# Optimization experiments

Hardware: AMD Instinct MI355X
Metric: run time of the kernel (lower is better)

The kernel has to match this reference:

```python
import jax, jax.numpy as jnp
import numpy as np

B, T, E, H, K, V = 64, 256, 300, 500, 64, 32000  # batch, seq, embed, hidden/dir, tags, vocab
PAD, EOS, SOS = 0, 1, 2
NEG = -10000.0


def setup_inputs() -> dict:
    key = jax.random.key(0)
    ks = jax.random.split(key, 20)
    rn = lambda k, shape, s=0.05: jax.random.normal(k, shape, jnp.float32) * s
    inp = {}
    inp["x"] = jax.random.randint(ks[0], (B, T), 3, V)   # all > 0 -> mask all ones (no padding)
    inp["y0"] = jax.random.randint(ks[1], (B, T), 3, K)  # gold tags, avoid PAD/EOS/SOS
    inp["embed"] = rn(ks[2], (V, E), 0.1)
    dims = [E, 2 * H]  # layer-0 input = embed, layer-1 input = concat(bi-dir hidden)
    i = 3
    for l in (0, 1):
        for d in ("f", "b"):
            inp[f"Wih{l}{d}"] = rn(ks[i], (4 * H, dims[l])); i += 1
            inp[f"Whh{l}{d}"] = rn(ks[i], (4 * H, H)); i += 1
            inp[f"b{l}{d}"] = rn(ks[i], (4 * H,)); i += 1
    inp["Wout"] = rn(ks[i], (K, 2 * H))
    inp["bout"] = rn(ks[i + 1], (K,))
    tr = jax.random.normal(ks[i + 2], (K, K), jnp.float32)
    tr = (tr.at[SOS, :].set(NEG).at[:, EOS].set(NEG).at[:, PAD].set(NEG)
            .at[PAD, :].set(NEG).at[PAD, EOS].set(0.0).at[PAD, PAD].set(0.0))
    inp["trans"] = tr  # trans[next, prev]
    return inp


def _lstm_dir(xs, Wih, Whh, b, reverse):
    """xs: [T,B,D] -> [T,B,H]; PyTorch gate order i,f,g,o."""
    if reverse:
        xs = xs[::-1]
    z0 = jnp.zeros((xs.shape[1], Whh.shape[1]), xs.dtype)

    def step(carry, xt):
        h, c = carry
        z = xt @ Wih.T + h @ Whh.T + b
        i_, f_, g_, o_ = jnp.split(z, 4, axis=-1)
        c = jax.nn.sigmoid(f_) * c + jax.nn.sigmoid(i_) * jnp.tanh(g_)
        h = jax.nn.sigmoid(o_) * jnp.tanh(c)
        return (h, c), h

    _, hs = jax.lax.scan(step, (z0, z0), xs)
    return hs[::-1] if reverse else hs


def reference(x, y0, embed, Wih0f, Whh0f, b0f, Wih0b, Whh0b, b0b,
              Wih1f, Whh1f, b1f, Wih1b, Whh1b, b1b, Wout, bout, trans):
    xs = embed[x].transpose(1, 0, 2)  # [T,B,E]
    h0 = jnp.concatenate([_lstm_dir(xs, Wih0f, Whh0f, b0f, False),
                          _lstm_dir(xs, Wih0b, Whh0b, b0b, True)], axis=-1)
    h1 = jnp.concatenate([_lstm_dir(h0, Wih1f, Whh1f, b1f, False),
                          _lstm_dir(h0, Wih1b, Whh1b, b1b, True)], axis=-1)
    emit = h1 @ Wout.T + bout                  # [T,B,K]
    mask = (x > 0).astype(emit.dtype).T        # [T,B]
    emit = emit * mask[..., None]              # y = y * mask

    # CRF partition (forward algorithm): new[b,j] = LSE_i(score[b,i] + trans[j,i]) + emit[t,b,j]
    init = jnp.full((B, K), NEG, emit.dtype).at[:, SOS].set(0.0)

    def step(score, em):
        e_t, m_t = em
        new = jax.nn.logsumexp(score[:, None, :] + trans[None, :, :], axis=-1) + e_t
        return jnp.where(m_t[:, None] > 0, new, score), None

    final, _ = jax.lax.scan(step, init, (emit, mask))
    Z = jax.nn.logsumexp(final, axis=-1)       # [B]

    # gold path score
    tags = jnp.concatenate([jnp.full((B, 1), SOS, y0.dtype), y0], axis=1)  # [B,T+1]
    e = jnp.take_along_axis(emit.transpose(1, 0, 2), tags[:, 1:, None], axis=2)[..., 0]  # [B,T]
    tr = trans[tags[:, 1:], tags[:, :-1]] * mask.T                                       # [B,T]
    gold = (e + tr).sum(axis=1)
    return Z - gold
```

## Files before the change

kernel.cpp:

```cpp
#include <hip/hip_runtime.h>
#include <hip/hip_bf16.h>

typedef short bf16x4 __attribute__((ext_vector_type(4)));
typedef short bf16x8 __attribute__((ext_vector_type(8)));
typedef float f32x4 __attribute__((ext_vector_type(4)));
typedef __hip_bfloat16 bf16;
typedef unsigned long long ull;

#define NEGV -10000.0f


__device__ __forceinline__ float sigm(float v) { return 1.0f / (1.0f + __expf(-v)); }
__device__ __forceinline__ float tanh_(float v) { float e = __expf(2.0f * v); return 1.0f - 2.0f / (e + 1.0f); }

__device__ __forceinline__ void async_load16(const bf16* g, const char* l) {
  __builtin_amdgcn_global_load_lds((const __attribute__((address_space(1))) void*)g,
                                   (__attribute__((address_space(3))) void*)l, 16, 0, 0);
}


__global__ __launch_bounds__(256) void pack_w0(const float* __restrict__ wf, const float* __restrict__ wb,
                                               bf16* __restrict__ dst) {
  int idx = blockIdx.x * 256 + threadIdx.x;
  int u = idx & 7, lane = (idx >> 3) & 63, rem = idx >> 9;
  int kt = rem % 10, nt = rem / 10;
  int n = (nt << 4) + (lane & 15), k = (kt << 5) + ((lane >> 4) << 3) + u;
  int d = n >> 11, g = (n >> 9) & 3, j = n & 511;
  float v = 0.f;
  if (j < 500 && k < 300) v = (d ? wb : wf)[(g * 500 + j) * 300 + k];
  dst[idx] = __float2bfloat16(v);
}

__global__ __launch_bounds__(256) void pack_whh4(const float* __restrict__ w0f, const float* __restrict__ w0b,
                                                 const float* __restrict__ w1f, const float* __restrict__ w1b,
                                                 bf16* __restrict__ dst) {
  const int which = blockIdx.y;
  const float* w = which == 0 ? w0f : which == 1 ? w0b : which == 2 ? w1f : w1b;
  int idx = blockIdx.x * 256 + threadIdx.x;
  int u = idx & 7, lane = (idx >> 3) & 63, rem = idx >> 9;
  int kt = rem & 15, nt = rem >> 4;
  int n = (nt << 4) + (lane & 15), k = (kt << 5) + ((lane >> 4) << 3) + u;
  int g = n >> 9, j = n & 511;
  float v = 0.f;
  if (j < 500 && k < 500) v = w[(g * 500 + j) * 500 + k];
  dst[(size_t)which * 1048576 + idx] = __float2bfloat16(v);
}

__global__ __launch_bounds__(256) void pack_w1(const float* __restrict__ wf, const float* __restrict__ wb,
                                               bf16* __restrict__ dst) {
  int idx = blockIdx.x * 256 + threadIdx.x;
  int u = idx & 7, lane = (idx >> 3) & 63, rem = idx >> 9;
  int kt = rem & 31, nt = rem >> 5;
  int n = (nt << 4) + (lane & 15), k = (kt << 5) + ((lane >> 4) << 3) + u;
  int d = n >> 11, g = (n >> 9) & 3, j = n & 511;
  int kk = k & 511;
  int ks = (k < 512) ? kk : 500 + kk;
  float v = 0.f;
  if (j < 500 && kk < 500) v = (d ? wb : wf)[(g * 500 + j) * 1000 + ks];
  dst[idx] = __float2bfloat16(v);
}

__global__ __launch_bounds__(256) void pack_wout(const float* __restrict__ w, bf16* __restrict__ dst) {
  int idx = blockIdx.x * 256 + threadIdx.x;
  int u = idx & 7, lane = (idx >> 3) & 63, rem = idx >> 9;
  int kt = rem & 31, nt = rem >> 5;
  int n = (nt << 4) + (lane & 15), k = (kt << 5) + ((lane >> 4) << 3) + u;
  int kk = k & 511;
  int ks = (k < 512) ? kk : 500 + kk;
  float v = 0.f;
  if (kk < 500) v = w[n * 1000 + ks];
  dst[idx] = __float2bfloat16(v);
}

__global__ __launch_bounds__(256) void pack_bias2(const float* __restrict__ b0f, const float* __restrict__ b0b,
                                                  const float* __restrict__ b1f, const float* __restrict__ b1b,
                                                  float* __restrict__ dst0, float* __restrict__ dst1) {
  int idx = blockIdx.x * 256 + threadIdx.x;
  int layer = idx >> 12, w = idx & 4095;
  int d = w >> 11, g = (w >> 9) & 3, j = w & 511;
  const float* src = layer ? (d ? b1b : b1f) : (d ? b0b : b0f);
  float v = (j < 500) ? src[g * 500 + j] : 0.f;
  (layer ? dst1 : dst0)[w] = v;
}

__global__ __launch_bounds__(256) void embed_k(const int* __restrict__ x, const float* __restrict__ em,
                                               bf16* __restrict__ xs) {
  int idx = blockIdx.x * 256 + threadIdx.x;
  int e = idx % 320;
  int row = idx / 320;
  int t = row >> 6, b = row & 63;
  float v = 0.f;
  if (e < 300) {
    int xv = x[b * 256 + t];
    v = em[(size_t)xv * 300 + e];
  }
  xs[idx] = __float2bfloat16(v);
}

__global__ __launch_bounds__(256) void gemm_nt(const bf16* __restrict__ A, const bf16* __restrict__ Bf,
                                               bf16* __restrict__ C, int Kdim, int Kt) {
  const int lane = threadIdx.x & 63, wave = threadIdx.x >> 6;
  const int lr = lane & 15, lh = lane >> 4;
  const int mb = blockIdx.x * 64;
  const int ntb = blockIdx.y * 16 + wave * 4;
  f32x4 acc[4][4] = {};
  for (int kt = 0; kt < Kt; ++kt) {
    bf16x8 a[4], b[4];
#pragma unroll
    for (int mt = 0; mt < 4; ++mt)
      a[mt] = *(const bf16x8*)(A + (size_t)(mb + mt * 16 + lr) * Kdim + kt * 32 + lh * 8);
#pragma unroll
    for (int q = 0; q < 4; ++q)
      b[q] = *(const bf16x8*)(Bf + ((size_t)(ntb + q) * Kt + kt) * 512 + lane * 8);
#pragma unroll
    for (int mt = 0; mt < 4; ++mt)
#pragma unroll
      for (int q = 0; q < 4; ++q)
        acc[mt][q] = __builtin_amdgcn_mfma_f32_16x16x32_bf16(a[mt], b[q], acc[mt][q], 0, 0, 0);
  }
  const int t = blockIdx.x;
#pragma unroll
  for (int q = 0; q < 4; ++q) {
    const int colbase = (ntb + q) * 16;
    const int dirq = colbase >> 11, gq = (colbase >> 9) & 3, jbq = (colbase >> 4) & 31;
    unsigned short vals[16];
#pragma unroll
    for (int mt = 0; mt < 4; ++mt)
#pragma unroll
      for (int r = 0; r < 4; ++r) {
        bf16 hb = __float2bfloat16(acc[mt][q][r]);
        vals[mt * 4 + r] = *(unsigned short*)&hb;
      }
    bf16* outp = C + ((((size_t)t * 2 + dirq) * 32 + jbq) * 4 + gq) * 1024 + lane * 16;
    *(bf16x8*)(outp) = *(const bf16x8*)(vals);
    *(bf16x8*)(outp + 8) = *(const bf16x8*)(vals + 8);
  }
}

__global__ __launch_bounds__(256, 1) void lstm_pipe(const bf16* __restrict__ preP, const bf16* __restrict__ whh,
                                                    const float* __restrict__ bias, bf16* __restrict__ hout,
                                                    unsigned int* __restrict__ flags) {
  constexpr int ROWS = 16;
  const int tid = threadIdx.x, lane = tid & 63, wave = tid >> 6;
  const int lr = lane & 15, lh = lane >> 4;
  const int jb = blockIdx.x, dir = blockIdx.y, part = blockIdx.z;
  unsigned int* flg = flags + (dir * 4 + part) * 64;
  unsigned int* myflg = flg + jb;
  __shared__ __align__(64) char hlds[4][16][1024];
  __shared__ float xch[4 * ROWS * 17];
  __shared__ float cst[ROWS * 16];
  for (int i = tid; i < ROWS * 16; i += 256) cst[i] = 0.f;
  const float bb = bias[dir * 2048 + wave * 512 + jb * 16 + lr];
  const bf16* wbase = whh + ((size_t)(dir * 128 + wave * 32 + jb) * 16) * 512 + lane * 8;

  bf16x8 wfrag[16];
#pragma unroll
  for (int kt = 0; kt < 16; ++kt) wfrag[kt] = *(const bf16x8*)(wbase + kt * 512);

  unsigned short pf[4];
  {
    const int t0 = dir ? 255 : 0;
    *(bf16x4*)pf = *(const bf16x4*)(preP + ((((size_t)t0 * 2 + dir) * 32 + jb) * 4 + wave) * 1024 +
                                    lane * 16 + part * 4);
  }

  const int srow_st = lane >> 2, sq_st = lane & 3;
  const int gchunk = (sq_st + ((srow_st >> 1) & 3)) & 3;
  const int rp = (lh - ((lr >> 1) & 3)) & 3;

  for (int s = 0; s < 256; ++s) {
    const int t = dir ? 255 - s : s;
    f32x4 acc = {};
    if (s > 0) {
      const unsigned int tgt = (unsigned int)s;
      const int tp = dir ? t + 1 : t - 1;
      const bf16* hp = hout + (size_t)tp * 65536 + dir * 512 +
                       (size_t)(part * 16 + srow_st) * 1024 + gchunk * 8;
      unsigned int pend = 0xFFFFu;
      while (pend) {
        unsigned int v = __hip_atomic_load(flg + (lane & 31), __ATOMIC_RELAXED, __HIP_MEMORY_SCOPE_AGENT);
        unsigned int am = (unsigned int)__ballot((int)(v >= tgt));
        unsigned int ready = 0;
#pragma unroll
        for (int j = 0; j < 16; ++j) {
          if (((pend >> j) & 1u) && (((am >> (2 * j)) & 3u) == 3u)) {
            async_load16(hp + j * 32, (const char*)&hlds[wave][j][0] + lane * 16);
            ready |= 1u << j;
          }
        }
        if (ready) {
          asm volatile("s_waitcnt vmcnt(0)" ::: "memory");
#pragma unroll
          for (int j = 0; j < 16; ++j) {
            if ((ready >> j) & 1u) {
              const bf16x8 afr = *(const bf16x8*)(&hlds[wave][j][0] + lr * 64 + rp * 16);
              acc = __builtin_amdgcn_mfma_f32_16x16x32_bf16(afr, wfrag[j], acc, 0, 0, 0);
            }
          }
          pend &= ~ready;
        }
      }
    }
#pragma unroll
    for (int r = 0; r < 4; ++r) {
      bf16 pv; *(unsigned short*)&pv = pf[r];
      xch[(wave * ROWS + lh * 4 + r) * 17 + lr] = acc[r] + bb + __bfloat162float(pv);
    }
    __syncthreads();
    if (tid < ROWS * 8) {
      const int row = tid >> 3, c0 = (tid & 7) * 2;
      unsigned int pk = 0;
#pragma unroll
      for (int i = 0; i < 2; ++i) {
        int col = c0 + i;
        float gi = xch[(0 * ROWS + row) * 17 + col];
        float gf = xch[(1 * ROWS + row) * 17 + col];
        float gg = xch[(2 * ROWS + row) * 17 + col];
        float go = xch[(3 * ROWS + row) * 17 + col];
        float c = cst[row * 16 + col];
        float cn = sigm(gf) * c + sigm(gi) * tanh_(gg);
        cst[row * 16 + col] = cn;
        bf16 hb = __float2bfloat16(sigm(go) * tanh_(cn));
        pk |= (unsigned int)(*(unsigned short*)&hb) << (16 * i);
      }
      unsigned int* hq =
          (unsigned int*)(hout + ((size_t)t * 64 + part * ROWS + row) * 1024 + dir * 512 + jb * 16 + c0);
      __hip_atomic_store(hq, pk, __ATOMIC_RELAXED, __HIP_MEMORY_SCOPE_AGENT);
    }
    asm volatile("s_waitcnt vmcnt(0)" ::: "memory");
    __syncthreads();
    if (tid == 0)
      __hip_atomic_store(myflg, (unsigned int)(s + 1), __ATOMIC_RELAXED, __HIP_MEMORY_SCOPE_AGENT);
    if (s < 255) {
      const int tn = dir ? t - 1 : t + 1;
      *(bf16x4*)pf = *(const bf16x4*)(preP + ((((size_t)tn * 2 + dir) * 32 + jb) * 4 + wave) * 1024 +
                                      lane * 16 + part * 4);
    }
  }
}

__global__ __launch_bounds__(256) void emit_k(const bf16* __restrict__ h1, const bf16* __restrict__ wo,
                                              const float* __restrict__ bout, const int* __restrict__ x,
                                              float* __restrict__ emit) {
  const int tid = threadIdx.x, lane = tid & 63, wave = tid >> 6;
  const int lr = lane & 15, lh = lane >> 4;
  const int mb = blockIdx.x * 64 + wave * 16;
  f32x4 acc[4] = {};
  for (int kt = 0; kt < 32; ++kt) {
    bf16x8 a = *(const bf16x8*)(h1 + (size_t)(mb + lr) * 1024 + kt * 32 + lh * 8);
#pragma unroll
    for (int q = 0; q < 4; ++q) {
      bf16x8 b = *(const bf16x8*)(wo + ((size_t)(q * 32 + kt) * 64 + lane) * 8);
      acc[q] = __builtin_amdgcn_mfma_f32_16x16x32_bf16(a, b, acc[q], 0, 0, 0);
    }
  }
#pragma unroll
  for (int q = 0; q < 4; ++q)
#pragma unroll
    for (int r = 0; r < 4; ++r) {
      int row = mb + lh * 4 + r;
      int col = q * 16 + lr;
      int tt = row >> 6, bi = row & 63;
      float m = (x[bi * 256 + tt] > 0) ? 1.f : 0.f;
      emit[(size_t)row * 64 + col] = (acc[q][r] + bout[col]) * m;
    }
}

__global__ __launch_bounds__(256) void crf_k(const float* __restrict__ emit, const float* __restrict__ trans,
                                             const int* __restrict__ x, const int* __restrict__ y0,
                                             float* __restrict__ out) {
  const int b = blockIdx.x, tid = threadIdx.x;
  __shared__ float tr[4096];
  __shared__ float sc[2][64];
  __shared__ float pm[4][64], ps[4][64];
  __shared__ float redw[4];
  for (int i = tid; i < 4096; i += 256) tr[i] = trans[i];
  if (tid < 64) sc[0][tid] = (tid == 2) ? 0.f : NEGV;
  __syncthreads();
  {
    const int t = tid;
    const int tag = y0[b * 256 + t];
    const int prev = t ? y0[b * 256 + t - 1] : 2;
    const float m = (x[b * 256 + t] > 0) ? 1.f : 0.f;
    float g = emit[((size_t)t * 64 + b) * 64 + tag] + tr[tag * 64 + prev] * m;
    for (int o = 32; o; o >>= 1) g += __shfl_down(g, o, 64);
    if ((tid & 63) == 0) redw[tid >> 6] = g;
  }
  __syncthreads();
  const float gold = redw[0] + redw[1] + redw[2] + redw[3];
  const int j = tid & 63, kq = tid >> 6;
  int cur = 0;
  for (int t = 0; t < 256; ++t) {
    const float* trj = tr + j * 64 + kq * 16;
    const float* scc = sc[cur] + kq * 16;
    float v[16];
    float mx = -3.0e38f;
#pragma unroll
    for (int k = 0; k < 16; ++k) {
      v[k] = scc[k] + trj[k];
      mx = fmaxf(mx, v[k]);
    }
    float sm = 0.f;
#pragma unroll
    for (int k = 0; k < 16; ++k) sm += __expf(v[k] - mx);
    pm[kq][j] = mx;
    ps[kq][j] = sm;
    __syncthreads();
    if (kq == 0) {
      float M = fmaxf(fmaxf(pm[0][j], pm[1][j]), fmaxf(pm[2][j], pm[3][j]));
      float S = ps[0][j] * __expf(pm[0][j] - M) + ps[1][j] * __expf(pm[1][j] - M) +
                ps[2][j] * __expf(pm[2][j] - M) + ps[3][j] * __expf(pm[3][j] - M);
      float nv = M + __logf(S) + emit[((size_t)t * 64 + b) * 64 + j];
      sc[cur ^ 1][j] = (x[b * 256 + t] > 0) ? nv : sc[cur][j];
    }
    __syncthreads();
    cur ^= 1;
  }
  if (tid < 64) {
    float v2 = sc[cur][tid];
    float M = v2;
    for (int o = 32; o; o >>= 1) M = fmaxf(M, __shfl_xor(M, o, 64));
    float s2 = __expf(v2 - M);
    for (int o = 32; o; o >>= 1) s2 += __shfl_xor(s2, o, 64);
    if (tid == 0) out[b] = M + __logf(s2) - gold;
  }
}

extern "C" void kernel_launch(void* const* d_in, const int* in_sizes, int n_in, void* d_out, int out_size,
                              void* d_ws, size_t ws_size, hipStream_t stream) {
  (void)in_sizes; (void)n_in; (void)out_size; (void)ws_size;
  const int* x = (const int*)d_in[0];
  const int* y0 = (const int*)d_in[1];
  const float* embed = (const float*)d_in[2];
  const float* Wih0f = (const float*)d_in[3];
  const float* Whh0f = (const float*)d_in[4];
  const float* b0f = (const float*)d_in[5];
  const float* Wih0b = (const float*)d_in[6];
  const float* Whh0b = (const float*)d_in[7];
  const float* b0b = (const float*)d_in[8];
  const float* Wih1f = (const float*)d_in[9];
  const float* Whh1f = (const float*)d_in[10];
  const float* b1f = (const float*)d_in[11];
  const float* Wih1b = (const float*)d_in[12];
  const float* Whh1b = (const float*)d_in[13];
  const float* b1b = (const float*)d_in[14];
  const float* Wout = (const float*)d_in[15];
  const float* bout = (const float*)d_in[16];
  const float* trans = (const float*)d_in[17];

  char* p = (char*)d_ws;
  auto take = [&](size_t n) { char* r = p; p += (n + 255) & ~(size_t)255; return r; };
  unsigned int* flags = (unsigned int*)take(2048 * sizeof(unsigned int));
  bf16* xs = (bf16*)take(16384ull * 320 * 2);
  bf16* preP = (bf16*)take(16384ull * 4096 * 2);
  bf16* h0 = (bf16*)take(16384ull * 1024 * 2);
  bf16* h1 = (bf16*)take(16384ull * 1024 * 2);
  float* emitb = (float*)take(16384ull * 64 * 4);
  bf16* W0B = (bf16*)take(4096ull * 320 * 2);
  bf16* W1B = (bf16*)take(4096ull * 1024 * 2);
  bf16* WhhB = (bf16*)take(4ull * 1048576 * 2);
  bf16* WoB = (bf16*)take(64ull * 1024 * 2);
  float* bias0 = (float*)take(4096 * 4);
  float* bias1 = (float*)take(4096 * 4);

  hipMemsetAsync(flags, 0, 2048 * sizeof(unsigned int), stream);
  hipLaunchKernelGGL(pack_w0, dim3(5120), dim3(256), 0, stream, Wih0f, Wih0b, W0B);
  hipLaunchKernelGGL(pack_whh4, dim3(4096, 4), dim3(256), 0, stream, Whh0f, Whh0b, Whh1f, Whh1b, WhhB);
  hipLaunchKernelGGL(pack_w1, dim3(16384), dim3(256), 0, stream, Wih1f, Wih1b, W1B);
  hipLaunchKernelGGL(pack_wout, dim3(256), dim3(256), 0, stream, Wout, WoB);
  hipLaunchKernelGGL(pack_bias2, dim3(32), dim3(256), 0, stream, b0f, b0b, b1f, b1b, bias0, bias1);
  hipLaunchKernelGGL(embed_k, dim3(20480), dim3(256), 0, stream, x, embed, xs);

  hipLaunchKernelGGL(gemm_nt, dim3(256, 16), dim3(256), 0, stream, xs, W0B, preP, 320, 10);
  {
    const bf16* a0 = preP; const bf16* a1 = WhhB; const float* a2 = bias0; bf16* a3 = h0;
    unsigned int* a4 = flags;
    void* args[] = {&a0, &a1, &a2, &a3, &a4};
    hipLaunchCooperativeKernel((void*)lstm_pipe, dim3(32, 2, 4), dim3(256), args, 0, stream);
  }
  hipLaunchKernelGGL(gemm_nt, dim3(256, 16), dim3(256), 0, stream, h0, W1B, preP, 1024, 32);
  {
    const bf16* a0 = preP; const bf16* a1 = WhhB + 2ull * 1048576; const float* a2 = bias1; bf16* a3 = h1;
    unsigned int* a4 = flags + 1024;
    void* args[] = {&a0, &a1, &a2, &a3, &a4};
    hipLaunchCooperativeKernel((void*)lstm_pipe, dim3(32, 2, 4), dim3(256), args, 0, stream);
  }
  hipLaunchKernelGGL(emit_k, dim3(256), dim3(256), 0, stream, h1, WoB, bout, x, emitb);
  hipLaunchKernelGGL(crf_k, dim3(64), dim3(256), 0, stream, emitb, trans, x, y0, (float*)d_out);
}
```

Measured before the change: 2.574 ms.

## Restructure LSTM recurrence so each wave owns a batch part with all gates

The recurrent LSTM kernel now has each wave handle one batch quarter and compute all four gates, instead of each wave computing one gate and exchanging results through shared memory. The recurrent weights move from registers into LDS, shared by the four waves, and the grid shrinks from 256 to 64 blocks. This removes the per-step block barriers and shared-memory gate exchange, and the cell update runs in registers with per-wave flag publication. In exchange each wave issues four times the MFMAs and reads weights from LDS every step, and fewer CUs are used.

```diff
diff --git a/kernel.cpp b/kernel.cpp
--- a/kernel.cpp
+++ b/kernel.cpp
@@ -137,32 +137,40 @@
   }
 }
 
-__global__ __launch_bounds__(256, 1) void lstm_pipe(const bf16* __restrict__ preP, const bf16* __restrict__ whh,
-                                                    const float* __restrict__ bias, bf16* __restrict__ hout,
-                                                    unsigned int* __restrict__ flags) {
-  constexpr int ROWS = 16;
+__global__ __launch_bounds__(256, 1) void lstm_wav(const bf16* __restrict__ preP, const bf16* __restrict__ whh,
+                                                   const float* __restrict__ bias, bf16* __restrict__ hout,
+                                                   unsigned int* __restrict__ flags) {
   const int tid = threadIdx.x, lane = tid & 63, wave = tid >> 6;
   const int lr = lane & 15, lh = lane >> 4;
-  const int jb = blockIdx.x, dir = blockIdx.y, part = blockIdx.z;
+  const int jb = blockIdx.x, dir = blockIdx.y, part = wave;
   unsigned int* flg = flags + (dir * 4 + part) * 64;
   unsigned int* myflg = flg + jb;
-  __shared__ __align__(64) char hlds[4][16][1024];
-  __shared__ float xch[4 * ROWS * 17];
-  __shared__ float cst[ROWS * 16];
-  for (int i = tid; i < ROWS * 16; i += 256) cst[i] = 0.f;
-  const float bb = bias[dir * 2048 + wave * 512 + jb * 16 + lr];
-  const bf16* wbase = whh + ((size_t)(dir * 128 + wave * 32 + jb) * 16) * 512 + lane * 8;
-
-  bf16x8 wfrag[16];
-#pragma unroll
-  for (int kt = 0; kt < 16; ++kt) wfrag[kt] = *(const bf16x8*)(wbase + kt * 512);
-
-  unsigned short pf[4];
+  __shared__ __align__(64) char wlds[4][16][1024];
+  __shared__ __align__(64) char hsl[4][16][1024];
+
+  {
+    const bf16* wsrc = whh + ((size_t)(dir * 128 + wave * 32 + jb) * 16) * 512 + lane * 8;
+#pragma unroll
+    for (int kt = 0; kt < 16; ++kt)
+      async_load16(wsrc + kt * 512, &wlds[wave][kt][0] + lane * 16);
+  }
+  asm volatile("s_waitcnt vmcnt(0)" ::: "memory");
+  __syncthreads();
+
+  float bb[4];
+#pragma unroll
+  for (int g = 0; g < 4; ++g) bb[g] = bias[dir * 2048 + g * 512 + jb * 16 + lr];
+
+  unsigned short pf[4][4];
   {
     const int t0 = dir ? 255 : 0;
-    *(bf16x4*)pf = *(const bf16x4*)(preP + ((((size_t)t0 * 2 + dir) * 32 + jb) * 4 + wave) * 1024 +
-                                    lane * 16 + part * 4);
-  }
+#pragma unroll
+    for (int g = 0; g < 4; ++g)
+      *(bf16x4*)pf[g] = *(const bf16x4*)(preP + ((((size_t)t0 * 2 + dir) * 32 + jb) * 4 + g) * 1024 +
+                                         lane * 16 + part * 4);
+  }
+
+  float cst[4] = {0.f, 0.f, 0.f, 0.f};
 
   const int srow_st = lane >> 2, sq_st = lane & 3;
   const int gchunk = (sq_st + ((srow_st >> 1) & 3)) & 3;
@@ -170,7 +178,7 @@
 
   for (int s = 0; s < 256; ++s) {
     const int t = dir ? 255 - s : s;
-    f32x4 acc = {};
+    f32x4 acc[4] = {};
     if (s > 0) {
       const unsigned int tgt = (unsigned int)s;
       const int tp = dir ? t + 1 : t - 1;
@@ -184,7 +192,7 @@
 #pragma unroll
         for (int j = 0; j < 16; ++j) {
           if (((pend >> j) & 1u) && (((am >> (2 * j)) & 3u) == 3u)) {
-            async_load16(hp + j * 32, (const char*)&hlds[wave][j][0] + lane * 16);
+            async_load16(hp + j * 32, &hsl[wave][j][0] + lane * 16);
             ready |= 1u << j;
           }
         }
@@ -193,8 +201,15 @@
 #pragma unroll
           for (int j = 0; j < 16; ++j) {
             if ((ready >> j) & 1u) {
-              const bf16x8 afr = *(const bf16x8*)(&hlds[wave][j][0] + lr * 64 + rp * 16);
-              acc = __builtin_amdgcn_mfma_f32_16x16x32_bf16(afr, wfrag[j], acc, 0, 0, 0);
+              const bf16x8 afr = *(const bf16x8*)(&hsl[wave][j][0] + lr * 64 + rp * 16);
+              acc[0] = __builtin_amdgcn_mfma_f32_16x16x32_bf16(
+                  afr, *(const bf16x8*)(&wlds[0][j][0] + lane * 16), acc[0], 0, 0, 0);
+              acc[1] = __builtin_amdgcn_mfma_f32_16x16x32_bf16(
+                  afr, *(const bf16x8*)(&wlds[1][j][0] + lane * 16), acc[1], 0, 0, 0);
+              acc[2] = __builtin_amdgcn_mfma_f32_16x16x32_bf16(
+                  afr, *(const bf16x8*)(&wlds[2][j][0] + lane * 16), acc[2], 0, 0, 0);
+              acc[3] = __builtin_amdgcn_mfma_f32_16x16x32_bf16(
+                  afr, *(const bf16x8*)(&wlds[3][j][0] + lane * 16), acc[3], 0, 0, 0);
             }
           }
           pend &= ~ready;
@@ -203,38 +218,31 @@
     }
 #pragma unroll
     for (int r = 0; r < 4; ++r) {
-      bf16 pv; *(unsigned short*)&pv = pf[r];
-      xch[(wave * ROWS + lh * 4 + r) * 17 + lr] = acc[r] + bb + __bfloat162float(pv);
-    }
-    __syncthreads();
-    if (tid < ROWS * 8) {
-      const int row = tid >> 3, c0 = (tid & 7) * 2;
-      unsigned int pk = 0;
-#pragma unroll
-      for (int i = 0; i < 2; ++i) {
-        int col = c0 + i;
-        float gi = xch[(0 * ROWS + row) * 17 + col];
-        float gf = xch[(1 * ROWS + row) * 17 + col];
-        float gg = xch[(2 * ROWS + row) * 17 + col];
-        float go = xch[(3 * ROWS + row) * 17 + col];
-        float c = cst[row * 16 + col];
-        float cn = sigm(gf) * c + sigm(gi) * tanh_(gg);
-        cst[row * 16 + col] = cn;
-        bf16 hb = __float2bfloat16(sigm(go) * tanh_(cn));
-        pk |= (unsigned int)(*(unsigned short*)&hb) << (16 * i);
-      }
-      unsigned int* hq =
-          (unsigned int*)(hout + ((size_t)t * 64 + part * ROWS + row) * 1024 + dir * 512 + jb * 16 + c0);
-      __hip_atomic_store(hq, pk, __ATOMIC_RELAXED, __HIP_MEMORY_SCOPE_AGENT);
+      bf16 p0, p1, p2, p3;
+      *(unsigned short*)&p0 = pf[0][r];
+      *(unsigned short*)&p1 = pf[1][r];
+      *(unsigned short*)&p2 = pf[2][r];
+      *(unsigned short*)&p3 = pf[3][r];
+      float gi = acc[0][r] + bb[0] + __bfloat162float(p0);
+      float gf = acc[1][r] + bb[1] + __bfloat162float(p1);
+      float gg = acc[2][r] + bb[2] + __bfloat162float(p2);
+      float go = acc[3][r] + bb[3] + __bfloat162float(p3);
+      float cn = sigm(gf) * cst[r] + sigm(gi) * tanh_(gg);
+      cst[r] = cn;
+      bf16 hb = __float2bfloat16(sigm(go) * tanh_(cn));
+      const bf16* addr = hout + ((size_t)t * 64 + part * 16 + lh * 4 + r) * 1024 + dir * 512 + jb * 16 + lr;
+      unsigned int hv = *(unsigned short*)&hb;
+      asm volatile("global_store_short %0, %1, off sc0 sc1" ::"v"(addr), "v"(hv) : "memory");
     }
     asm volatile("s_waitcnt vmcnt(0)" ::: "memory");
-    __syncthreads();
-    if (tid == 0)
+    if (lane == 0)
       __hip_atomic_store(myflg, (unsigned int)(s + 1), __ATOMIC_RELAXED, __HIP_MEMORY_SCOPE_AGENT);
     if (s < 255) {
       const int tn = dir ? t - 1 : t + 1;
-      *(bf16x4*)pf = *(const bf16x4*)(preP + ((((size_t)tn * 2 + dir) * 32 + jb) * 4 + wave) * 1024 +
-                                      lane * 16 + part * 4);
+#pragma unroll
+      for (int g = 0; g < 4; ++g)
+        *(bf16x4*)pf[g] = *(const bf16x4*)(preP + ((((size_t)tn * 2 + dir) * 32 + jb) * 4 + g) * 1024 +
+                                           lane * 16 + part * 4);
     }
   }
 }
@@ -376,14 +384,14 @@
     const bf16* a0 = preP; const bf16* a1 = WhhB; const float* a2 = bias0; bf16* a3 = h0;
     unsigned int* a4 = flags;
     void* args[] = {&a0, &a1, &a2, &a3, &a4};
-    hipLaunchCooperativeKernel((void*)lstm_pipe, dim3(32, 2, 4), dim3(256), args, 0, stream);
+    hipLaunchCooperativeKernel((void*)lstm_wav, dim3(32, 2), dim3(256), args, 0, stream);
   }
   hipLaunchKernelGGL(gemm_nt, dim3(256, 16), dim3(256), 0, stream, h0, W1B, preP, 1024, 32);
   {
     const bf16* a0 = preP; const bf16* a1 = WhhB + 2ull * 1048576; const float* a2 = bias1; bf16* a3 = h1;
     unsigned int* a4 = flags + 1024;
     void* args[] = {&a0, &a1, &a2, &a3, &a4};
-    hipLaunchCooperativeKernel((void*)lstm_pipe, dim3(32, 2, 4), dim3(256), args, 0, stream);
+    hipLaunchCooperativeKernel((void*)lstm_wav, dim3(32, 2), dim3(256), args, 0, stream);
   }
   hipLaunchKernelGGL(emit_k, dim3(256), dim3(256), 0, stream, h1, WoB, bout, x, emitb);
   hipLaunchKernelGGL(crf_k, dim3(64), dim3(256), 0, stream, emitb, trans, x, y0, (float*)d_out);
```

Measured after the change: 3.554 ms. +38.1%, slower.
